# Kernel optimization log

Hardware: AMD Instinct MI355X
Metric: run time of the kernel (lower is better)

Reference implementation:

```python
import jax, jax.numpy as jnp
from jax import lax
import numpy as np

KERNEL = 3
PAD = KERNEL // 2


def _normalized_weights(affinity):
    # affinity: [B, 8, H, W] -> 9-tap weights [B, 9, H, W] with center at index 4
    aff_sum = jnp.sum(jnp.abs(affinity), axis=1, keepdims=True)
    aff_norm = affinity / aff_sum
    center = 1.0 - jnp.sum(aff_norm, axis=1, keepdims=True)
    # Original loop uses affinity channels 0..3 for taps before center, 4..7 after
    return jnp.concatenate([aff_norm[:, :4], center, aff_norm[:, 4:]], axis=1)


def setup_inputs() -> dict:
    key = jax.random.key(0)
    k1, k2 = jax.random.split(key)
    B, H, W = 8, 480, 640
    affinity = jax.random.normal(k1, (B, KERNEL * KERNEL - 1, H, W), dtype=jnp.float32)
    feature = jax.random.normal(k2, (B, 1, H, W), dtype=jnp.float32)
    return {"affinity": affinity, "feature": feature, "times": 24}


def reference(affinity, feature, times):
    weights = _normalized_weights(affinity)  # [B, 9, H, W]
    B, C, H, W = feature.shape

    def step(f, _):
        fp = jnp.pad(f, ((0, 0), (0, 0), (PAD, PAD), (PAD, PAD)))
        # 9 shifted views stacked on a tap axis: [B, 9, C, H, W]
        shifts = jnp.stack(
            [fp[:, :, i:i + H, j:j + W] for i in range(KERNEL) for j in range(KERNEL)],
            axis=1,
        )
        f_new = jnp.sum(shifts * weights[:, :, None, :, :], axis=1)
        return f_new, None

    out, _ = lax.scan(step, feature, None, length=times)
    return out
```

## Files before the change

### kernel.cpp

```cpp
#include <hip/hip_runtime.h>
#include <hip/hip_fp16.h>
#include <cstddef>


#define HIMG 480
#define WIMG 640
#define HW   (HIMG * WIMG)
#define BN   8

#define TILE   40
#define TSTEPS 12
#define IH     13
#define WHL    12
#define SW     66
#define PITCH  68
#define NT     512

#define WS_FRAME_B  ((size_t)BN * HW * 4)
#define WS_WA_B     ((size_t)BN * HW * 16)
#define WS_WC_B     ((size_t)BN * HW * 4)
#define WS_NEED     (WS_FRAME_B + WS_WA_B + WS_WC_B)

template <int MODE>
__global__ __launch_bounds__(NT, 4) void affprop12(
    const float* __restrict__ aff,
    __half2* __restrict__ wA,
    float* __restrict__ wC,
    const float* __restrict__ src,
    float* __restrict__ dst)
{
    __shared__ float fA[SW * PITCH];
    __shared__ float fB[SW * PITCH];

    const int tid = threadIdx.x;
    const int ox  = blockIdx.x * TILE;
    const int oy  = blockIdx.y * TILE;
    const int b   = blockIdx.z;

    const float* __restrict__ sb = src + (size_t)b * HW;
    float*       __restrict__ db = dst + (size_t)b * HW;

    for (int i = tid; i < SW * SW; i += NT) {
        int r  = i / SW;
        int c  = i - r * SW;
        int gy = oy - IH + r;
        int gx = ox - IH + c;
        float v = 0.f;
        if ((unsigned)gy < (unsigned)HIMG && (unsigned)gx < (unsigned)WIMG)
            v = sb[gy * WIMG + gx];
        fA[r * PITCH + c] = v;
    }
    for (int i = tid; i < SW * PITCH / 4; i += NT)
        *(float4*)&fB[4 * i] = make_float4(0.f, 0.f, 0.f, 0.f);

    const int c  = tid & 63;
    const int g  = tid >> 6;
    const int sc = c + 1;

    __half2 wv[8][4];
    float   wcc[8];

    #pragma unroll
    for (int i = 0; i < 8; ++i) {
        const int gy = oy - WHL + 8 * g + i;
        const int gx = ox - WHL + c;
        const bool in = (unsigned)gy < (unsigned)HIMG && (unsigned)gx < (unsigned)WIMG;
        const size_t idx = (size_t)b * HW + (size_t)gy * WIMG + gx;

        if (MODE == 1) {
            if (in) {
                union { float4 f4; __half2 h[4]; } u;
                u.f4 = *(const float4*)(wA + 4 * idx);
                wv[i][0] = u.h[0]; wv[i][1] = u.h[1];
                wv[i][2] = u.h[2]; wv[i][3] = u.h[3];
                wcc[i] = wC[idx];
            } else {
                __half2 z = __floats2half2_rn(0.f, 0.f);
                wv[i][0] = z; wv[i][1] = z; wv[i][2] = z; wv[i][3] = z;
                wcc[i] = 0.f;
            }
        } else {
            float w[8];
            float s = 0.f;
            if (in) {
                const float* ap = aff + (size_t)b * 8 * HW + (size_t)gy * WIMG + gx;
                #pragma unroll
                for (int k = 0; k < 8; ++k) { w[k] = ap[(size_t)k * HW]; s += fabsf(w[k]); }
            } else {
                #pragma unroll
                for (int k = 0; k < 8; ++k) w[k] = 0.f;
                s = 1.f;
            }
            float rr  = in ? 1.0f / s : 0.f;
            float acc = 0.f;
            #pragma unroll
            for (int k = 0; k < 8; ++k) { w[k] *= rr; acc += w[k]; }

            union { float4 f4; __half2 h[4]; } u;
            u.h[0] = __floats2half2_rn(w[0], w[1]);
            u.h[1] = __floats2half2_rn(w[2], w[3]);
            u.h[2] = __floats2half2_rn(w[4], w[5]);
            u.h[3] = __floats2half2_rn(w[6], w[7]);
            wv[i][0] = u.h[0]; wv[i][1] = u.h[1];
            wv[i][2] = u.h[2]; wv[i][3] = u.h[3];
            wcc[i] = in ? 1.0f - acc : 0.f;

            if (MODE == 0) {
                if ((unsigned)(gy - oy) < (unsigned)TILE &&
                    (unsigned)(gx - ox) < (unsigned)TILE) {
                    *(float4*)(wA + 4 * idx) = u.f4;
                    wC[idx] = wcc[i];
                }
            }
        }
    }
    __syncthreads();

    const float* fin = fA;
    float*       fo  = fB;

    #pragma unroll 1
    for (int s = 0; s < TSTEPS; ++s) {
        const bool live = (8 * g + 8 >= s + 1) && (8 * g + 1 <= 64 - s);
        if (live) {
            const float* bp = fin + (8 * g) * PITCH + c;
            float t0[10], t1[10], t2[10];
            #pragma unroll
            for (int r = 0; r < 10; ++r) {
                t0[r] = bp[r * PITCH + 0];
                t1[r] = bp[r * PITCH + 1];
                t2[r] = bp[r * PITCH + 2];
            }
            float* wp = fo + (8 * g + 1) * PITCH + sc;
            #pragma unroll
            for (int i = 0; i < 8; ++i) {
                float o = wcc[i] * t1[i + 1]
                    + __low2float (wv[i][0]) * t0[i]
                    + __high2float(wv[i][0]) * t1[i]
                    + __low2float (wv[i][1]) * t2[i]
                    + __high2float(wv[i][1]) * t0[i + 1]
                    + __low2float (wv[i][2]) * t2[i + 1]
                    + __high2float(wv[i][2]) * t0[i + 2]
                    + __low2float (wv[i][3]) * t1[i + 2]
                    + __high2float(wv[i][3]) * t2[i + 2];
                wp[i * PITCH] = o;
            }
        }
        __syncthreads();
        const float* t = fin; fin = fo; fo = (float*)t;
    }

    for (int i = tid; i < TILE * (TILE / 4); i += NT) {
        int r  = i / (TILE / 4);
        int c4 = (i - r * (TILE / 4)) * 4;
        const float* p = fin + (IH + r) * PITCH + IH + c4;
        float4 v = make_float4(p[0], p[1], p[2], p[3]);
        *(float4*)&db[(size_t)(oy + r) * WIMG + ox + c4] = v;
    }
}

extern "C" void kernel_launch(void* const* d_in, const int* in_sizes, int n_in,
                              void* d_out, int out_size, void* d_ws, size_t ws_size,
                              hipStream_t stream)
{
    const float* aff  = (const float*)d_in[0];
    const float* feat = (const float*)d_in[1];
    float* out = (float*)d_out;

    char* ws = (char*)d_ws;
    float*   wsFrame = (float*)ws;
    __half2* wA      = (__half2*)(ws + WS_FRAME_B);
    float*   wC      = (float*)(ws + WS_FRAME_B + WS_WA_B);

    dim3 blk(NT, 1, 1);
    dim3 grd(WIMG / TILE, HIMG / TILE, BN);

    if (ws_size >= WS_NEED) {
        affprop12<0><<<grd, blk, 0, stream>>>(aff, wA, wC, feat, wsFrame);
        affprop12<1><<<grd, blk, 0, stream>>>(aff, wA, wC, wsFrame, out);
    } else {
        affprop12<2><<<grd, blk, 0, stream>>>(aff, nullptr, nullptr, feat, wsFrame);
        affprop12<2><<<grd, blk, 0, stream>>>(aff, nullptr, nullptr, wsFrame, out);
    }
}
```

Before: 214.7 us.

## Fuse two propagation steps per barrier using wavefront shuffles for intermediate

Each thread now computes an intermediate step for 10 rows, recomputing a halo row above and below. The second step takes its horizontal neighbours through wavefront lane shuffles instead of shared memory, so only every other step is written to LDS and synchronised. This halves the barrier and LDS round-trip count, at the cost of redundant halo computation, more weight registers (10 rows instead of 8), and edge lanes whose shuffled neighbours are invalid, which lowers the useful width of each wavefront.

```diff
diff --git a/kernel.cpp b/kernel.cpp
--- a/kernel.cpp
+++ b/kernel.cpp
@@ -10,9 +10,11 @@
 
 #define TILE   40
 #define TSTEPS 12
+#define NPER   6
 #define IH     13
 #define WHL    12
 #define SW     66
+#define ROWS   68
 #define PITCH  68
 #define NT     512
 
@@ -29,8 +31,8 @@
     const float* __restrict__ src,
     float* __restrict__ dst)
 {
-    __shared__ float fA[SW * PITCH];
-    __shared__ float fB[SW * PITCH];
+    __shared__ float fA[ROWS * PITCH];
+    __shared__ float fB[ROWS * PITCH];
 
     const int tid = threadIdx.x;
     const int ox  = blockIdx.x * TILE;
@@ -48,21 +50,26 @@
         float v = 0.f;
         if ((unsigned)gy < (unsigned)HIMG && (unsigned)gx < (unsigned)WIMG)
             v = sb[gy * WIMG + gx];
-        fA[r * PITCH + c] = v;
-    }
-    for (int i = tid; i < SW * PITCH / 4; i += NT)
+        fA[(r + 1) * PITCH + c] = v;
+    }
+    for (int i = tid; i < 2 * PITCH; i += NT) {
+        int r = (i < PITCH) ? 0 : (ROWS - 1);
+        int c = (i < PITCH) ? i : i - PITCH;
+        fA[r * PITCH + c] = 0.f;
+    }
+    for (int i = tid; i < ROWS * PITCH / 4; i += NT)
         *(float4*)&fB[4 * i] = make_float4(0.f, 0.f, 0.f, 0.f);
 
     const int c  = tid & 63;
     const int g  = tid >> 6;
     const int sc = c + 1;
 
-    __half2 wv[8][4];
-    float   wcc[8];
+    __half2 wv[10][4];
+    float   wcc[10];
 
     #pragma unroll
-    for (int i = 0; i < 8; ++i) {
-        const int gy = oy - WHL + 8 * g + i;
+    for (int j = 0; j < 10; ++j) {
+        const int gy = oy - WHL + 8 * g - 1 + j;
         const int gx = ox - WHL + c;
         const bool in = (unsigned)gy < (unsigned)HIMG && (unsigned)gx < (unsigned)WIMG;
         const size_t idx = (size_t)b * HW + (size_t)gy * WIMG + gx;
@@ -71,13 +78,13 @@
             if (in) {
                 union { float4 f4; __half2 h[4]; } u;
                 u.f4 = *(const float4*)(wA + 4 * idx);
-                wv[i][0] = u.h[0]; wv[i][1] = u.h[1];
-                wv[i][2] = u.h[2]; wv[i][3] = u.h[3];
-                wcc[i] = wC[idx];
+                wv[j][0] = u.h[0]; wv[j][1] = u.h[1];
+                wv[j][2] = u.h[2]; wv[j][3] = u.h[3];
+                wcc[j] = wC[idx];
             } else {
                 __half2 z = __floats2half2_rn(0.f, 0.f);
-                wv[i][0] = z; wv[i][1] = z; wv[i][2] = z; wv[i][3] = z;
-                wcc[i] = 0.f;
+                wv[j][0] = z; wv[j][1] = z; wv[j][2] = z; wv[j][3] = z;
+                wcc[j] = 0.f;
             }
         } else {
             float w[8];
@@ -101,15 +108,16 @@
             u.h[1] = __floats2half2_rn(w[2], w[3]);
             u.h[2] = __floats2half2_rn(w[4], w[5]);
             u.h[3] = __floats2half2_rn(w[6], w[7]);
-            wv[i][0] = u.h[0]; wv[i][1] = u.h[1];
-            wv[i][2] = u.h[2]; wv[i][3] = u.h[3];
-            wcc[i] = in ? 1.0f - acc : 0.f;
+            wv[j][0] = u.h[0]; wv[j][1] = u.h[1];
+            wv[j][2] = u.h[2]; wv[j][3] = u.h[3];
+            wcc[j] = in ? 1.0f - acc : 0.f;
 
             if (MODE == 0) {
-                if ((unsigned)(gy - oy) < (unsigned)TILE &&
+                if (j >= 1 && j <= 8 &&
+                    (unsigned)(gy - oy) < (unsigned)TILE &&
                     (unsigned)(gx - ox) < (unsigned)TILE) {
                     *(float4*)(wA + 4 * idx) = u.f4;
-                    wC[idx] = wcc[i];
+                    wC[idx] = wcc[j];
                 }
             }
         }
@@ -120,29 +128,48 @@
     float*       fo  = fB;
 
     #pragma unroll 1
-    for (int s = 0; s < TSTEPS; ++s) {
-        const bool live = (8 * g + 8 >= s + 1) && (8 * g + 1 <= 64 - s);
+    for (int p = 0; p < NPER; ++p) {
+        const bool live = (8 * g + 8 >= 2 * p + 2) && (8 * g + 1 <= 63 - 2 * p);
         if (live) {
             const float* bp = fin + (8 * g) * PITCH + c;
-            float t0[10], t1[10], t2[10];
-            #pragma unroll
-            for (int r = 0; r < 10; ++r) {
-                t0[r] = bp[r * PITCH + 0];
-                t1[r] = bp[r * PITCH + 1];
-                t2[r] = bp[r * PITCH + 2];
-            }
-            float* wp = fo + (8 * g + 1) * PITCH + sc;
+            float u0[12], u1[12], u2[12];
+            #pragma unroll
+            for (int k = 0; k < 12; ++k) {
+                u0[k] = bp[k * PITCH + 0];
+                u1[k] = bp[k * PITCH + 1];
+                u2[k] = bp[k * PITCH + 2];
+            }
+            float m[10];
+            #pragma unroll
+            for (int j = 0; j < 10; ++j) {
+                m[j] = wcc[j] * u1[j + 1]
+                    + __low2float (wv[j][0]) * u0[j]
+                    + __high2float(wv[j][0]) * u1[j]
+                    + __low2float (wv[j][1]) * u2[j]
+                    + __high2float(wv[j][1]) * u0[j + 1]
+                    + __low2float (wv[j][2]) * u2[j + 1]
+                    + __high2float(wv[j][2]) * u0[j + 2]
+                    + __low2float (wv[j][3]) * u1[j + 2]
+                    + __high2float(wv[j][3]) * u2[j + 2];
+            }
+            float mL[10], mR[10];
+            #pragma unroll
+            for (int j = 0; j < 10; ++j) {
+                mL[j] = __shfl_up(m[j], 1);
+                mR[j] = __shfl_down(m[j], 1);
+            }
+            float* wp = fo + (8 * g + 2) * PITCH + sc;
             #pragma unroll
             for (int i = 0; i < 8; ++i) {
-                float o = wcc[i] * t1[i + 1]
-                    + __low2float (wv[i][0]) * t0[i]
-                    + __high2float(wv[i][0]) * t1[i]
-                    + __low2float (wv[i][1]) * t2[i]
-                    + __high2float(wv[i][1]) * t0[i + 1]
-                    + __low2float (wv[i][2]) * t2[i + 1]
-                    + __high2float(wv[i][2]) * t0[i + 2]
-                    + __low2float (wv[i][3]) * t1[i + 2]
-                    + __high2float(wv[i][3]) * t2[i + 2];
+                float o = wcc[i + 1] * m[i + 1]
+                    + __low2float (wv[i + 1][0]) * mL[i]
+                    + __high2float(wv[i + 1][0]) * m[i]
+                    + __low2float (wv[i + 1][1]) * mR[i]
+                    + __high2float(wv[i + 1][1]) * mL[i + 1]
+                    + __low2float (wv[i + 1][2]) * mR[i + 1]
+                    + __high2float(wv[i + 1][2]) * mL[i + 2]
+                    + __low2float (wv[i + 1][3]) * m[i + 2]
+                    + __high2float(wv[i + 1][3]) * mR[i + 2];
                 wp[i * PITCH] = o;
             }
         }
@@ -153,7 +180,7 @@
     for (int i = tid; i < TILE * (TILE / 4); i += NT) {
         int r  = i / (TILE / 4);
         int c4 = (i - r * (TILE / 4)) * 4;
-        const float* p = fin + (IH + r) * PITCH + IH + c4;
+        const float* p = fin + (IH + 1 + r) * PITCH + IH + c4;
         float4 v = make_float4(p[0], p[1], p[2], p[3]);
         *(float4*)&db[(size_t)(oy + r) * WIMG + ox + c4] = v;
     }
```

Measured after the change: 220.9 us. 1.03x slower.

## Switch per-thread stencil footprint to 4x2 output blocks with float2 LDS loads

Applied to the files above, without the earlier changes.

Each thread now computes a 4-row by 2-column patch instead of an 8-row by 1-column strip, loading a 6x4 window from LDS with float2 reads. The aim is fewer LDS instructions per output (24 floats read per 8 outputs instead of 30) and wider vectorized shared-memory access. The liveness test still works on whole wavefronts, but the halo overlap is now in both dimensions. The float2 access pattern at even offsets could also change bank-conflict behaviour.

```diff
diff --git a/kernel.cpp b/kernel.cpp
--- a/kernel.cpp
+++ b/kernel.cpp
@@ -53,63 +53,67 @@
     for (int i = tid; i < SW * PITCH / 4; i += NT)
         *(float4*)&fB[4 * i] = make_float4(0.f, 0.f, 0.f, 0.f);
 
-    const int c  = tid & 63;
-    const int g  = tid >> 6;
-    const int sc = c + 1;
+    const int cu = tid & 31;
+    const int rg = tid >> 5;
+    const int w  = tid >> 6;
 
-    __half2 wv[8][4];
-    float   wcc[8];
+    __half2 wv[4][2][4];
+    float   wcc[4][2];
 
     #pragma unroll
-    for (int i = 0; i < 8; ++i) {
-        const int gy = oy - WHL + 8 * g + i;
-        const int gx = ox - WHL + c;
-        const bool in = (unsigned)gy < (unsigned)HIMG && (unsigned)gx < (unsigned)WIMG;
-        const size_t idx = (size_t)b * HW + (size_t)gy * WIMG + gx;
+    for (int i = 0; i < 4; ++i) {
+        #pragma unroll
+        for (int k = 0; k < 2; ++k) {
+            const int gy = oy - WHL + 4 * rg + i;
+            const int gx = ox - WHL + 2 * cu + k;
+            const bool in = (unsigned)gy < (unsigned)HIMG && (unsigned)gx < (unsigned)WIMG;
+            const size_t idx = (size_t)b * HW + (size_t)gy * WIMG + gx;
 
-        if (MODE == 1) {
-            if (in) {
+            if (MODE == 1) {
+                if (in) {
+                    union { float4 f4; __half2 h[4]; } u;
+                    u.f4 = *(const float4*)(wA + 4 * idx);
+                    wv[i][k][0] = u.h[0]; wv[i][k][1] = u.h[1];
+                    wv[i][k][2] = u.h[2]; wv[i][k][3] = u.h[3];
+                    wcc[i][k] = wC[idx];
+                } else {
+                    __half2 z = __floats2half2_rn(0.f, 0.f);
+                    wv[i][k][0] = z; wv[i][k][1] = z;
+                    wv[i][k][2] = z; wv[i][k][3] = z;
+                    wcc[i][k] = 0.f;
+                }
+            } else {
+                float wt[8];
+                float s = 0.f;
+                if (in) {
+                    const float* ap = aff + (size_t)b * 8 * HW + (size_t)gy * WIMG + gx;
+                    #pragma unroll
+                    for (int t = 0; t < 8; ++t) { wt[t] = ap[(size_t)t * HW]; s += fabsf(wt[t]); }
+                } else {
+                    #pragma unroll
+                    for (int t = 0; t < 8; ++t) wt[t] = 0.f;
+                    s = 1.f;
+                }
+                float rr  = in ? 1.0f / s : 0.f;
+                float acc = 0.f;
+                #pragma unroll
+                for (int t = 0; t < 8; ++t) { wt[t] *= rr; acc += wt[t]; }
+
                 union { float4 f4; __half2 h[4]; } u;
-                u.f4 = *(const float4*)(wA + 4 * idx);
-                wv[i][0] = u.h[0]; wv[i][1] = u.h[1];
-                wv[i][2] = u.h[2]; wv[i][3] = u.h[3];
-                wcc[i] = wC[idx];
-            } else {
-                __half2 z = __floats2half2_rn(0.f, 0.f);
-                wv[i][0] = z; wv[i][1] = z; wv[i][2] = z; wv[i][3] = z;
-                wcc[i] = 0.f;
-            }
-        } else {
-            float w[8];
-            float s = 0.f;
-            if (in) {
-                const float* ap = aff + (size_t)b * 8 * HW + (size_t)gy * WIMG + gx;
-                #pragma unroll
-                for (int k = 0; k < 8; ++k) { w[k] = ap[(size_t)k * HW]; s += fabsf(w[k]); }
-            } else {
-                #pragma unroll
-                for (int k = 0; k < 8; ++k) w[k] = 0.f;
-                s = 1.f;
-            }
-            float rr  = in ? 1.0f / s : 0.f;
-            float acc = 0.f;
-            #pragma unroll
-            for (int k = 0; k < 8; ++k) { w[k] *= rr; acc += w[k]; }
+                u.h[0] = __floats2half2_rn(wt[0], wt[1]);
+                u.h[1] = __floats2half2_rn(wt[2], wt[3]);
+                u.h[2] = __floats2half2_rn(wt[4], wt[5]);
+                u.h[3] = __floats2half2_rn(wt[6], wt[7]);
+                wv[i][k][0] = u.h[0]; wv[i][k][1] = u.h[1];
+                wv[i][k][2] = u.h[2]; wv[i][k][3] = u.h[3];
+                wcc[i][k] = in ? 1.0f - acc : 0.f;
 
-            union { float4 f4; __half2 h[4]; } u;
-            u.h[0] = __floats2half2_rn(w[0], w[1]);
-            u.h[1] = __floats2half2_rn(w[2], w[3]);
-            u.h[2] = __floats2half2_rn(w[4], w[5]);
-            u.h[3] = __floats2half2_rn(w[6], w[7]);
-            wv[i][0] = u.h[0]; wv[i][1] = u.h[1];
-            wv[i][2] = u.h[2]; wv[i][3] = u.h[3];
-            wcc[i] = in ? 1.0f - acc : 0.f;
-
-            if (MODE == 0) {
-                if ((unsigned)(gy - oy) < (unsigned)TILE &&
-                    (unsigned)(gx - ox) < (unsigned)TILE) {
-                    *(float4*)(wA + 4 * idx) = u.f4;
-                    wC[idx] = wcc[i];
+                if (MODE == 0) {
+                    if ((unsigned)(gy - oy) < (unsigned)TILE &&
+                        (unsigned)(gx - ox) < (unsigned)TILE) {
+                        *(float4*)(wA + 4 * idx) = u.f4;
+                        wC[idx] = wcc[i][k];
+                    }
                 }
             }
         }
@@ -121,29 +125,37 @@
 
     #pragma unroll 1
     for (int s = 0; s < TSTEPS; ++s) {
-        const bool live = (8 * g + 8 >= s + 1) && (8 * g + 1 <= 64 - s);
+        const bool live = (8 * w + 8 >= s + 1) && (8 * w + 1 <= 64 - s);
         if (live) {
-            const float* bp = fin + (8 * g) * PITCH + c;
-            float t0[10], t1[10], t2[10];
+            const float* bp = fin + (4 * rg) * PITCH + 2 * cu;
+            float2 p0[6], p1[6];
             #pragma unroll
-            for (int r = 0; r < 10; ++r) {
-                t0[r] = bp[r * PITCH + 0];
-                t1[r] = bp[r * PITCH + 1];
-                t2[r] = bp[r * PITCH + 2];
+            for (int r = 0; r < 6; ++r) {
+                p0[r] = *(const float2*)(bp + r * PITCH);
+                p1[r] = *(const float2*)(bp + r * PITCH + 2);
             }
-            float* wp = fo + (8 * g + 1) * PITCH + sc;
+            float Wm[6][4];
             #pragma unroll
-            for (int i = 0; i < 8; ++i) {
-                float o = wcc[i] * t1[i + 1]
-                    + __low2float (wv[i][0]) * t0[i]
-                    + __high2float(wv[i][0]) * t1[i]
-                    + __low2float (wv[i][1]) * t2[i]
-                    + __high2float(wv[i][1]) * t0[i + 1]
-                    + __low2float (wv[i][2]) * t2[i + 1]
-                    + __high2float(wv[i][2]) * t0[i + 2]
-                    + __low2float (wv[i][3]) * t1[i + 2]
-                    + __high2float(wv[i][3]) * t2[i + 2];
-                wp[i * PITCH] = o;
+            for (int r = 0; r < 6; ++r) {
+                Wm[r][0] = p0[r].x; Wm[r][1] = p0[r].y;
+                Wm[r][2] = p1[r].x; Wm[r][3] = p1[r].y;
+            }
+            float* wp = fo + (4 * rg + 1) * PITCH + (2 * cu + 1);
+            #pragma unroll
+            for (int i = 0; i < 4; ++i) {
+                #pragma unroll
+                for (int k = 0; k < 2; ++k) {
+                    float o = wcc[i][k] * Wm[i + 1][k + 1]
+                        + __low2float (wv[i][k][0]) * Wm[i][k]
+                        + __high2float(wv[i][k][0]) * Wm[i][k + 1]
+                        + __low2float (wv[i][k][1]) * Wm[i][k + 2]
+                        + __high2float(wv[i][k][1]) * Wm[i + 1][k]
+                        + __low2float (wv[i][k][2]) * Wm[i + 1][k + 2]
+                        + __high2float(wv[i][k][2]) * Wm[i + 2][k]
+                        + __low2float (wv[i][k][3]) * Wm[i + 2][k + 1]
+                        + __high2float(wv[i][k][3]) * Wm[i + 2][k + 2];
+                    wp[i * PITCH + k] = o;
+                }
             }
         }
         __syncthreads();
```

Measured after the change: 232.4 us. 1.08x slower.
